# Kernel optimization log

Hardware: AMD Instinct MI355X
Metric: run time of the kernel (lower is better)

Reference implementation:

```python
import jax, jax.numpy as jnp
import numpy as np

K = 1024
DIM = 64
DECAY = 0.99
EPS = 1e-05
CC = 0.25


def setup_inputs() -> dict:
    key = jax.random.key(0)
    k1, k2 = jax.random.split(key)
    inputs = jax.random.normal(k1, (32, DIM, 64, 64), dtype=jnp.float32)
    # embedding initialized uniform(-1/K, 1/K); ema_w starts as a copy
    emb_w = jax.random.uniform(k2, (K, DIM), dtype=jnp.float32, minval=-1.0 / K, maxval=1.0 / K)
    ema_w = emb_w
    ema_cluster_size = jnp.zeros((K,), dtype=jnp.float32)
    return {"inputs": inputs, "emb_w": emb_w, "ema_cluster_size": ema_cluster_size, "ema_w": ema_w}


def reference(inputs, emb_w, ema_cluster_size, ema_w):
    # NCHW -> NHWC
    x = jnp.transpose(inputs, (0, 2, 3, 1))  # [B,H,W,D]
    B, H, W, D = x.shape
    flat = x.reshape(-1, D)  # [N,D]
    # squared L2 distances: |f|^2 - 2 f.W^T + |w|^2
    d = (jnp.sum(flat * flat, axis=1, keepdims=True)
         - 2.0 * flat @ emb_w.T
         + jnp.sum(emb_w * emb_w, axis=1)[None, :])  # [N,K]
    idx = jnp.argmin(d, axis=1)  # [N]
    encodings = idx.reshape(B, H, W)
    quantized = emb_w[idx].reshape(B, H, W, D)

    # training-mode EMA update (matches one_hot.sum(0) and one_hot.T @ flatten)
    counts = jax.ops.segment_sum(jnp.ones_like(idx, dtype=jnp.float32), idx, num_segments=K)
    new_cs = ema_cluster_size * DECAY + (1.0 - DECAY) * counts
    n = jnp.sum(new_cs)
    new_cs = (new_cs + EPS) / (n + K * EPS) * n
    dw = jax.ops.segment_sum(flat, idx, num_segments=K)  # [K,D]
    new_ema_w = ema_w * DECAY + (1.0 - DECAY) * dw
    new_emb_w = new_ema_w / new_cs[:, None]

    e_latent_loss = jnp.mean((quantized - x) ** 2)  # both terms equal in value
    loss = e_latent_loss + CC * e_latent_loss
    # straight-through (value-equal in fwd)
    q_out = jnp.transpose(quantized, (0, 3, 1, 2))  # NHWC -> NCHW
    nll = jnp.ones((1,), dtype=jnp.float32)
    return q_out, encodings, loss, nll, new_cs, new_ema_w, new_emb_w
```

## Files before the change

### kernel.cpp

```cpp
#include <hip/hip_runtime.h>
#include <math.h>

#define KCODES 1024
#define DIMV   64
#define NROWS  131072
#define HWSZ   4096
#define NELEM  8388608
#define CAP    224
#define CANDCAP 1024
#define RPB    128


typedef __attribute__((ext_vector_type(8))) short bf16x8;
typedef __attribute__((ext_vector_type(4))) float f32x4;

static __device__ __forceinline__ unsigned short f2bf(float x) {
    unsigned int u = __float_as_uint(x);
    unsigned int r = (u + 0x7FFFu + ((u >> 16) & 1u)) >> 16;
    return (unsigned short)r;
}

__global__ __launch_bounds__(64) void vq_prep3_kernel(
    const float* __restrict__ emb, float* __restrict__ s_w,
    unsigned short* __restrict__ WB, unsigned int* __restrict__ wmax_bits)
{
    int k = blockIdx.x, t = threadIdx.x;
    float v = emb[k * DIMV + t];

    {
        int cg = k >> 4, n = k & 15;
        int kh = t >> 5, q = (t & 31) >> 3, j = t & 7;
        WB[((cg * 2 + kh) * 4 + q) * 128 + n * 8 + j] = f2bf(v);
    }

    float av = fabsf(v);
    #pragma unroll
    for (int off = 32; off > 0; off >>= 1)
        av = fmaxf(av, __shfl_down(av, off, 64));
    if (t == 0) atomicMax(wmax_bits, __float_as_uint(av));

    __shared__ float sv[64];
    __shared__ float sr[8];
    sv[t] = v;
    __syncthreads();
    if (t < 8) {
        float x = sv[t];
        float sq = x * x;
        asm("" : "+v"(sq));
        float r = sq;
        #pragma unroll
        for (int m = 1; m < 8; ++m) {
            float y = sv[8 * m + t];
            float s2 = y * y;
            asm("" : "+v"(s2));
            r += s2;
        }
        sr[t] = r;
    }
    __syncthreads();
    if (t == 0)
        s_w[k] = ((sr[0] + sr[1]) + (sr[2] + sr[3])) + ((sr[4] + sr[5]) + (sr[6] + sr[7]));
}

__global__ __launch_bounds__(256, 3) void vq_assign_kernel(
    const float* __restrict__ inp, const float* __restrict__ emb,
    const unsigned short* __restrict__ WB, const float* __restrict__ s_w,
    const unsigned int* __restrict__ wmax_bits,
    float* __restrict__ tmp_flat, float* __restrict__ enc_out,
    double* __restrict__ loss_sum, int* __restrict__ counts,
    int* __restrict__ rowlist)
{
    __shared__ float At[RPB * 65];
    __shared__ float sWL[KCODES];
    __shared__ __align__(16) unsigned short Bst[2][2048];
    __shared__ float sfL[RPB];
    __shared__ float errL[RPB];
    __shared__ unsigned long long rowBest[RPB];
    __shared__ int bkL[RPB];
    __shared__ int candL[CANDCAP];
    __shared__ int candCnt;

    const int t = threadIdx.x;
    const int n0 = blockIdx.x * RPB;
    const int bq  = n0 >> 12;
    const int hw0 = n0 & 4095;
    const float* fin = inp + (size_t)bq * (DIMV * HWSZ) + hw0;

    if (t < RPB) rowBest[t] = ~0ULL;
    if (t == 0) candCnt = 0;

    #pragma unroll
    for (int j = 0; j < 4; ++j) sWL[j * 256 + t] = s_w[j * 256 + t];

    #pragma unroll
    for (int j = 0; j < 8; ++j) {
        int id = j * 256 + t;
        int i = id >> 5;
        int c4 = id & 31;
        float4 v = *(const float4*)(fin + (size_t)i * HWSZ + 4 * c4);
        int r = 4 * c4;
        At[(r + 0) * 65 + i] = v.x + v.x;  At[(r + 1) * 65 + i] = v.y + v.y;
        At[(r + 2) * 65 + i] = v.z + v.z;  At[(r + 3) * 65 + i] = v.w + v.w;
    }

    const uint4* wbsrc = (const uint4*)WB;
    uint4 nx0, nx1;
    {
        uint4 st0 = wbsrc[t];
        *(uint4*)&Bst[0][t * 8] = st0;
        nx0 = wbsrc[256 + t];
    }
    __syncthreads();

    if (t < RPB) {
        const float* gr = &At[t * 65];
        float r8[8];
        #pragma unroll
        for (int j = 0; j < 8; ++j) {
            float h = 0.5f * gr[j];
            float sq = h * h;
            asm("" : "+v"(sq));
            r8[j] = sq;
        }
        #pragma unroll
        for (int m = 1; m < 8; ++m) {
            #pragma unroll
            for (int j = 0; j < 8; ++j) {
                float h = 0.5f * gr[8 * m + j];
                float sq = h * h;
                asm("" : "+v"(sq));
                r8[j] += sq;
            }
        }
        sfL[t] = ((r8[0] + r8[1]) + (r8[2] + r8[3])) + ((r8[4] + r8[5]) + (r8[6] + r8[7]));
        float S = 0.0f;
        #pragma unroll
        for (int i = 0; i < 64; ++i) S += fabsf(gr[i]);
        float wmax = __uint_as_float(*wmax_bits);
        errL[t] = fmaf(S * wmax, 0.015625f, 2e-5f);
    }
    __syncthreads();

    const int wv = t >> 6, l = t & 63;
    const int m = l & 15, q = l >> 4;
    const int lq = q * 128 + m * 8;
    bf16x8 afr[2][2];
    float erf[2][4];
    #pragma unroll
    for (int rg2 = 0; rg2 < 2; ++rg2) {
        int row = (2 * wv + rg2) * 16 + m;
        const float* gr = &At[row * 65];
        #pragma unroll
        for (int kh = 0; kh < 2; ++kh) {
            bf16x8 a;
            #pragma unroll
            for (int j = 0; j < 8; ++j)
                a[j] = (short)f2bf(gr[kh * 32 + q * 8 + j]);
            afr[rg2][kh] = a;
        }
        #pragma unroll
        for (int reg = 0; reg < 4; ++reg)
            erf[rg2][reg] = errL[(2 * wv + rg2) * 16 + q * 4 + reg];
    }

    float mn[2][4];
    #pragma unroll
    for (int rg2 = 0; rg2 < 2; ++rg2)
        #pragma unroll
        for (int reg = 0; reg < 4; ++reg) mn[rg2][reg] = 3.0e38f;

    #pragma unroll 1
    for (int tp = 0; tp < 16; ++tp) {
        int tt = 2 * tp;
        nx1 = wbsrc[((tt + 2) & 31) * 256 + t];
        #pragma unroll
        for (int c = 0; c < 2; ++c) {
            int cg = 2 * tt + c;
            bf16x8 b0 = *(const bf16x8*)&Bst[0][c * 1024 + lq];
            bf16x8 b1 = *(const bf16x8*)&Bst[0][c * 1024 + 512 + lq];
            float sw = sWL[cg * 16 + m];
            #pragma unroll
            for (int rg2 = 0; rg2 < 2; ++rg2) {
                f32x4 acc = {0.f, 0.f, 0.f, 0.f};
                acc = __builtin_amdgcn_mfma_f32_16x16x32_bf16(afr[rg2][0], b0, acc, 0, 0, 0);
                acc = __builtin_amdgcn_mfma_f32_16x16x32_bf16(afr[rg2][1], b1, acc, 0, 0, 0);
                #pragma unroll
                for (int reg = 0; reg < 4; ++reg)
                    mn[rg2][reg] = fminf(mn[rg2][reg], sw - acc[reg]);
            }
        }
        *(uint4*)&Bst[1][t * 8] = nx0;
        __syncthreads();
        nx0 = wbsrc[((tt + 3) & 31) * 256 + t];
        #pragma unroll
        for (int c = 0; c < 2; ++c) {
            int cg = 2 * (tt + 1) + c;
            bf16x8 b0 = *(const bf16x8*)&Bst[1][c * 1024 + lq];
            bf16x8 b1 = *(const bf16x8*)&Bst[1][c * 1024 + 512 + lq];
            float sw = sWL[cg * 16 + m];
            #pragma unroll
            for (int rg2 = 0; rg2 < 2; ++rg2) {
                f32x4 acc = {0.f, 0.f, 0.f, 0.f};
                acc = __builtin_amdgcn_mfma_f32_16x16x32_bf16(afr[rg2][0], b0, acc, 0, 0, 0);
                acc = __builtin_amdgcn_mfma_f32_16x16x32_bf16(afr[rg2][1], b1, acc, 0, 0, 0);
                #pragma unroll
                for (int reg = 0; reg < 4; ++reg)
                    mn[rg2][reg] = fminf(mn[rg2][reg], sw - acc[reg]);
            }
        }
        *(uint4*)&Bst[0][t * 8] = nx1;
        __syncthreads();
    }

    float th[2][4];
    #pragma unroll
    for (int rg2 = 0; rg2 < 2; ++rg2)
        #pragma unroll
        for (int reg = 0; reg < 4; ++reg) {
            float v = mn[rg2][reg];
            v = fminf(v, __shfl_xor(v, 1, 64));
            v = fminf(v, __shfl_xor(v, 2, 64));
            v = fminf(v, __shfl_xor(v, 4, 64));
            v = fminf(v, __shfl_xor(v, 8, 64));
            th[rg2][reg] = v + erf[rg2][reg];
        }

    #pragma unroll 1
    for (int tp = 0; tp < 16; ++tp) {
        int tt = 2 * tp;
        nx1 = wbsrc[((tt + 2) & 31) * 256 + t];
        #pragma unroll
        for (int c = 0; c < 2; ++c) {
            int cg = 2 * tt + c;
            bf16x8 b0 = *(const bf16x8*)&Bst[0][c * 1024 + lq];
            bf16x8 b1 = *(const bf16x8*)&Bst[0][c * 1024 + 512 + lq];
            float sw = sWL[cg * 16 + m];
            #pragma unroll
            for (int rg2 = 0; rg2 < 2; ++rg2) {
                f32x4 acc = {0.f, 0.f, 0.f, 0.f};
                acc = __builtin_amdgcn_mfma_f32_16x16x32_bf16(afr[rg2][0], b0, acc, 0, 0, 0);
                acc = __builtin_amdgcn_mfma_f32_16x16x32_bf16(afr[rg2][1], b1, acc, 0, 0, 0);
                #pragma unroll
                for (int reg = 0; reg < 4; ++reg) {
                    if (sw - acc[reg] <= th[rg2][reg]) {
                        int row = (2 * wv + rg2) * 16 + q * 4 + reg;
                        int p = atomicAdd(&candCnt, 1);
                        if (p < CANDCAP) candL[p] = (row << 10) | (cg * 16 + m);
                    }
                }
            }
        }
        *(uint4*)&Bst[1][t * 8] = nx0;
        __syncthreads();
        nx0 = wbsrc[((tt + 3) & 31) * 256 + t];
        #pragma unroll
        for (int c = 0; c < 2; ++c) {
            int cg = 2 * (tt + 1) + c;
            bf16x8 b0 = *(const bf16x8*)&Bst[1][c * 1024 + lq];
            bf16x8 b1 = *(const bf16x8*)&Bst[1][c * 1024 + 512 + lq];
            float sw = sWL[cg * 16 + m];
            #pragma unroll
            for (int rg2 = 0; rg2 < 2; ++rg2) {
                f32x4 acc = {0.f, 0.f, 0.f, 0.f};
                acc = __builtin_amdgcn_mfma_f32_16x16x32_bf16(afr[rg2][0], b0, acc, 0, 0, 0);
                acc = __builtin_amdgcn_mfma_f32_16x16x32_bf16(afr[rg2][1], b1, acc, 0, 0, 0);
                #pragma unroll
                for (int reg = 0; reg < 4; ++reg) {
                    if (sw - acc[reg] <= th[rg2][reg]) {
                        int row = (2 * wv + rg2) * 16 + q * 4 + reg;
                        int p = atomicAdd(&candCnt, 1);
                        if (p < CANDCAP) candL[p] = (row << 10) | (cg * 16 + m);
                    }
                }
            }
        }
        *(uint4*)&Bst[0][t * 8] = nx1;
        __syncthreads();
    }

    int nc = candCnt < CANDCAP ? candCnt : CANDCAP;
    for (int c = t; c < nc; c += 256) {
        int pk = candL[c];
        int r = pk >> 10, k = pk & 1023;
        const float* wk = emb + (size_t)k * DIMV;
        const float* gr = &At[r * 65];
        float acc = 0.0f;
        #pragma unroll
        for (int i = 0; i < DIMV; ++i)
            acc = __builtin_fmaf(gr[i], wk[i], acc);
        float d = (sfL[r] - acc) + sWL[k];
        unsigned int u = __float_as_uint(d);
        unsigned int s = (u & 0x80000000u) ? ~u : (u | 0x80000000u);
        unsigned long long key = ((unsigned long long)s << 32) | (unsigned int)k;
        atomicMin(&rowBest[r], key);
    }
    __syncthreads();

    if (t < RPB && (rowBest[t] == ~0ULL || candCnt > CANDCAP)) {
        int r = t;
        const float* gr = &At[r * 65];
        float bd = 3.0e38f; int bk = 0;
        for (int k = 0; k < KCODES; ++k) {
            const float* wk = emb + (size_t)k * DIMV;
            float acc = 0.0f;
            #pragma unroll
            for (int i = 0; i < DIMV; ++i)
                acc = __builtin_fmaf(gr[i], wk[i], acc);
            float d = (sfL[r] - acc) + sWL[k];
            if (d < bd) { bd = d; bk = k; }
        }
        unsigned int u = __float_as_uint(bd);
        unsigned int s = (u & 0x80000000u) ? ~u : (u | 0x80000000u);
        rowBest[r] = ((unsigned long long)s << 32) | (unsigned int)bk;
    }
    __syncthreads();

    if (t < RPB) {
        int r = t;
        int bk = (int)(rowBest[r] & 1023ULL);
        enc_out[n0 + r] = (float)bk;
        bkL[r] = bk;
        int pos = atomicAdd(&counts[bk], 1);
        if (pos < CAP) rowlist[bk * CAP + pos] = n0 + r;
    }
    __syncthreads();

    float* tq = tmp_flat + (size_t)n0 * DIMV;
    double lsum = 0.0;
    #pragma unroll
    for (int j = 0; j < 32; ++j) {
        int idx = j * 256 + t;
        int r = idx >> 6;
        int i = idx & 63;
        int bk = bkL[r];
        float fi = 0.5f * At[r * 65 + i];
        tq[r * DIMV + i] = fi;
        float qv = emb[bk * DIMV + i];
        double dq = (double)qv - (double)fi;
        lsum = fma(dq, dq, lsum);
    }
    #pragma unroll
    for (int off = 32; off > 0; off >>= 1)
        lsum += __shfl_down(lsum, off, 64);
    if ((t & 63) == 0) atomicAdd(loss_sum, lsum);
}

__global__ __launch_bounds__(256) void vq_dw_all_kernel(
    const float* __restrict__ tmp_flat, const int* __restrict__ rowlist,
    const int* __restrict__ counts, const float* __restrict__ ema_cs,
    const float* __restrict__ ema_w, const double* __restrict__ loss_sum,
    float* __restrict__ out_loss, float* __restrict__ out_nll,
    float* __restrict__ out_ncs, float* __restrict__ out_nema,
    float* __restrict__ out_nemb)
{
    const int k = blockIdx.x;
    const int t = threadIdx.x;
    const double DECAY = 0.99;
    const double OMD   = 1.0 - 0.99;
    const double EPSV  = 1e-5;

    __shared__ double sm[256];
    double part = 0.0;
    #pragma unroll
    for (int j0 = 0; j0 < 4; ++j0) {
        int j = j0 * 256 + t;
        part += (double)ema_cs[j] * DECAY + OMD * (double)counts[j];
    }
    sm[t] = part;
    __syncthreads();
    #pragma unroll
    for (int off = 128; off > 0; off >>= 1) {
        if (t < off) sm[t] += sm[t + off];
        __syncthreads();
    }
    double nsum = sm[0];

    int cnt = counts[k];
    double ncs = (double)ema_cs[k] * DECAY + OMD * (double)cnt;
    double adj = (ncs + EPSV) / (nsum + (double)KCODES * EPSV) * nsum;
    if (t == 0) out_ncs[k] = (float)adj;
    if (k == 0 && t == 0) {
        double e = loss_sum[0] / (double)NELEM;
        out_loss[0] = (float)(e + 0.25 * e);
        out_nll[0]  = 1.0f;
    }

    int i = t & 63;
    int sub = t >> 6;
    int cap = cnt < CAP ? cnt : CAP;

    float acc = 0.0f;
    #pragma unroll 4
    for (int r = sub; r < cap; r += 4) {
        int n = rowlist[k * CAP + r];
        acc += tmp_flat[(size_t)n * DIMV + i];
    }

    __shared__ float red[256];
    red[t] = acc;
    __syncthreads();
    if (t < 128) red[t] += red[t + 128];
    __syncthreads();
    if (t < 64) {
        float dwv = red[t] + red[t + 64];
        int idx = k * DIMV + i;
        double ne = (double)ema_w[idx] * DECAY + OMD * (double)dwv;
        out_nema[idx] = (float)ne;
        out_nemb[idx] = (float)(ne / adj);
    }
}

__global__ __launch_bounds__(256) void vq_qout_kernel(
    const float* __restrict__ enc, const float* __restrict__ emb,
    float* __restrict__ q_out)
{
    __shared__ int bkL[128];
    const int t = threadIdx.x;
    const int n0 = blockIdx.x * 128;
    const int bq  = n0 >> 12;
    const int hw0 = n0 & 4095;
    if (t < 128) bkL[t] = (int)enc[n0 + t];
    __syncthreads();
    float* qo = q_out + (size_t)bq * (DIMV * HWSZ) + hw0;
    #pragma unroll
    for (int j = 0; j < 32; ++j) {
        int idx = j * 256 + t;
        int r = idx & 127;
        int i = idx >> 7;
        qo[(size_t)i * HWSZ + r] = emb[bkL[r] * DIMV + i];
    }
}

extern "C" void kernel_launch(void* const* d_in, const int* in_sizes, int n_in,
                              void* d_out, int out_size, void* d_ws, size_t ws_size,
                              hipStream_t stream) {
    const float* inp    = (const float*)d_in[0];
    const float* emb    = (const float*)d_in[1];
    const float* ema_cs = (const float*)d_in[2];
    const float* ema_w  = (const float*)d_in[3];

    char* ws = (char*)d_ws;
    double*         loss_sum  = (double*)(ws + 0);
    unsigned int*   wmax_bits = (unsigned int*)(ws + 16);
    int*            counts    = (int*)(ws + 32);
    float*          s_w       = (float*)(ws + 4128);
    unsigned short* WB        = (unsigned short*)(ws + 8224);
    int*            rowlist   = (int*)(ws + 139296);

    float* out       = (float*)d_out;
    float* q_out     = out;
    float* enc_out   = out + 8388608;
    float* out_loss  = out + 8519680;
    float* out_nll   = out + 8519681;
    float* out_ncs   = out + 8519682;
    float* out_nema  = out + 8520706;
    float* out_nemb  = out + 8586242;

    hipMemsetAsync(ws, 0, 4128, stream);
    hipLaunchKernelGGL(vq_prep3_kernel, dim3(KCODES), dim3(64), 0, stream,
                       emb, s_w, WB, wmax_bits);
    hipLaunchKernelGGL(vq_assign_kernel, dim3(NROWS / RPB), dim3(256), 0, stream,
                       inp, emb, WB, s_w, wmax_bits,
                       q_out , enc_out, loss_sum, counts, rowlist);
    hipLaunchKernelGGL(vq_dw_all_kernel, dim3(KCODES), dim3(256), 0, stream,
                       q_out , rowlist, counts, ema_cs, ema_w, loss_sum,
                       out_loss, out_nll, out_ncs, out_nema, out_nemb);
    hipLaunchKernelGGL(vq_qout_kernel, dim3(NROWS / 128), dim3(256), 0, stream,
                       enc_out, emb, q_out);
}
```

Measured before the change: 266.4 us.

## Stream codebook tiles with direct global-to-LDS loads and interleave MFMAs

```diff
diff --git a/kernel.cpp b/kernel.cpp
--- a/kernel.cpp
+++ b/kernel.cpp
@@ -13,6 +13,10 @@
 
 typedef __attribute__((ext_vector_type(8))) short bf16x8;
 typedef __attribute__((ext_vector_type(4))) float f32x4;
+
+#define GLD16(gsrc, ldst) __builtin_amdgcn_global_load_lds( \
+    (const __attribute__((address_space(1))) void*)(gsrc),  \
+    (__attribute__((address_space(3))) void*)(ldst), 16, 0, 0)
 
 static __device__ __forceinline__ unsigned short f2bf(float x) {
     unsigned int u = __float_as_uint(x);
@@ -92,6 +96,9 @@
     #pragma unroll
     for (int j = 0; j < 4; ++j) sWL[j * 256 + t] = s_w[j * 256 + t];
 
+    const char* wbByte = (const char*)WB;
+    GLD16(wbByte + t * 16, (char*)&Bst[0][0] + t * 16);
+
     #pragma unroll
     for (int j = 0; j < 8; ++j) {
         int id = j * 256 + t;
@@ -102,14 +109,6 @@
         At[(r + 0) * 65 + i] = v.x + v.x;  At[(r + 1) * 65 + i] = v.y + v.y;
         At[(r + 2) * 65 + i] = v.z + v.z;  At[(r + 3) * 65 + i] = v.w + v.w;
     }
-
-    const uint4* wbsrc = (const uint4*)WB;
-    uint4 nx0, nx1;
-    {
-        uint4 st0 = wbsrc[t];
-        *(uint4*)&Bst[0][t * 8] = st0;
-        nx0 = wbsrc[256 + t];
-    }
     __syncthreads();
 
     if (t < RPB) {
@@ -170,45 +169,33 @@
         for (int reg = 0; reg < 4; ++reg) mn[rg2][reg] = 3.0e38f;
 
     #pragma unroll 1
-    for (int tp = 0; tp < 16; ++tp) {
-        int tt = 2 * tp;
-        nx1 = wbsrc[((tt + 2) & 31) * 256 + t];
-        #pragma unroll
-        for (int c = 0; c < 2; ++c) {
-            int cg = 2 * tt + c;
-            bf16x8 b0 = *(const bf16x8*)&Bst[0][c * 1024 + lq];
-            bf16x8 b1 = *(const bf16x8*)&Bst[0][c * 1024 + 512 + lq];
-            float sw = sWL[cg * 16 + m];
-            #pragma unroll
-            for (int rg2 = 0; rg2 < 2; ++rg2) {
-                f32x4 acc = {0.f, 0.f, 0.f, 0.f};
-                acc = __builtin_amdgcn_mfma_f32_16x16x32_bf16(afr[rg2][0], b0, acc, 0, 0, 0);
-                acc = __builtin_amdgcn_mfma_f32_16x16x32_bf16(afr[rg2][1], b1, acc, 0, 0, 0);
-                #pragma unroll
-                for (int reg = 0; reg < 4; ++reg)
-                    mn[rg2][reg] = fminf(mn[rg2][reg], sw - acc[reg]);
-            }
-        }
-        *(uint4*)&Bst[1][t * 8] = nx0;
-        __syncthreads();
-        nx0 = wbsrc[((tt + 3) & 31) * 256 + t];
-        #pragma unroll
-        for (int c = 0; c < 2; ++c) {
-            int cg = 2 * (tt + 1) + c;
-            bf16x8 b0 = *(const bf16x8*)&Bst[1][c * 1024 + lq];
-            bf16x8 b1 = *(const bf16x8*)&Bst[1][c * 1024 + 512 + lq];
-            float sw = sWL[cg * 16 + m];
-            #pragma unroll
-            for (int rg2 = 0; rg2 < 2; ++rg2) {
-                f32x4 acc = {0.f, 0.f, 0.f, 0.f};
-                acc = __builtin_amdgcn_mfma_f32_16x16x32_bf16(afr[rg2][0], b0, acc, 0, 0, 0);
-                acc = __builtin_amdgcn_mfma_f32_16x16x32_bf16(afr[rg2][1], b1, acc, 0, 0, 0);
-                #pragma unroll
-                for (int reg = 0; reg < 4; ++reg)
-                    mn[rg2][reg] = fminf(mn[rg2][reg], sw - acc[reg]);
-            }
-        }
-        *(uint4*)&Bst[0][t * 8] = nx1;
+    for (int tp = 0; tp < 32; ++tp) {
+        int nxt = (tp + 1) & 31;
+        GLD16(wbByte + nxt * 4096 + t * 16, (char*)&Bst[(tp + 1) & 1][0] + t * 16);
+        const unsigned short* bb = &Bst[tp & 1][0];
+        bf16x8 b00 = *(const bf16x8*)&bb[lq];
+        bf16x8 b01 = *(const bf16x8*)&bb[512 + lq];
+        bf16x8 b10 = *(const bf16x8*)&bb[1024 + lq];
+        bf16x8 b11 = *(const bf16x8*)&bb[1536 + lq];
+        float sw0 = sWL[(2 * tp) * 16 + m];
+        float sw1 = sWL[(2 * tp + 1) * 16 + m];
+        f32x4 t00 = {0.f,0.f,0.f,0.f}, t10 = {0.f,0.f,0.f,0.f};
+        f32x4 t01 = {0.f,0.f,0.f,0.f}, t11 = {0.f,0.f,0.f,0.f};
+        t00 = __builtin_amdgcn_mfma_f32_16x16x32_bf16(afr[0][0], b00, t00, 0, 0, 0);
+        t10 = __builtin_amdgcn_mfma_f32_16x16x32_bf16(afr[1][0], b00, t10, 0, 0, 0);
+        t01 = __builtin_amdgcn_mfma_f32_16x16x32_bf16(afr[0][0], b10, t01, 0, 0, 0);
+        t11 = __builtin_amdgcn_mfma_f32_16x16x32_bf16(afr[1][0], b10, t11, 0, 0, 0);
+        t00 = __builtin_amdgcn_mfma_f32_16x16x32_bf16(afr[0][1], b01, t00, 0, 0, 0);
+        t10 = __builtin_amdgcn_mfma_f32_16x16x32_bf16(afr[1][1], b01, t10, 0, 0, 0);
+        t01 = __builtin_amdgcn_mfma_f32_16x16x32_bf16(afr[0][1], b11, t01, 0, 0, 0);
+        t11 = __builtin_amdgcn_mfma_f32_16x16x32_bf16(afr[1][1], b11, t11, 0, 0, 0);
+        #pragma unroll
+        for (int reg = 0; reg < 4; ++reg) {
+            mn[0][reg] = fminf(mn[0][reg], sw0 - t00[reg]);
+            mn[1][reg] = fminf(mn[1][reg], sw0 - t10[reg]);
+            mn[0][reg] = fminf(mn[0][reg], sw1 - t01[reg]);
+            mn[1][reg] = fminf(mn[1][reg], sw1 - t11[reg]);
+        }
         __syncthreads();
     }
 
@@ -226,55 +213,50 @@
         }
 
     #pragma unroll 1
-    for (int tp = 0; tp < 16; ++tp) {
-        int tt = 2 * tp;
-        nx1 = wbsrc[((tt + 2) & 31) * 256 + t];
-        #pragma unroll
-        for (int c = 0; c < 2; ++c) {
-            int cg = 2 * tt + c;
-            bf16x8 b0 = *(const bf16x8*)&Bst[0][c * 1024 + lq];
-            bf16x8 b1 = *(const bf16x8*)&Bst[0][c * 1024 + 512 + lq];
-            float sw = sWL[cg * 16 + m];
-            #pragma unroll
-            for (int rg2 = 0; rg2 < 2; ++rg2) {
-                f32x4 acc = {0.f, 0.f, 0.f, 0.f};
-                acc = __builtin_amdgcn_mfma_f32_16x16x32_bf16(afr[rg2][0], b0, acc, 0, 0, 0);
-                acc = __builtin_amdgcn_mfma_f32_16x16x32_bf16(afr[rg2][1], b1, acc, 0, 0, 0);
-                #pragma unroll
-                for (int reg = 0; reg < 4; ++reg) {
-                    if (sw - acc[reg] <= th[rg2][reg]) {
-                        int row = (2 * wv + rg2) * 16 + q * 4 + reg;
-                        int p = atomicAdd(&candCnt, 1);
-                        if (p < CANDCAP) candL[p] = (row << 10) | (cg * 16 + m);
-                    }
-                }
+    for (int tp = 0; tp < 32; ++tp) {
+        int nxt = (tp + 1) & 31;
+        GLD16(wbByte + nxt * 4096 + t * 16, (char*)&Bst[(tp + 1) & 1][0] + t * 16);
+        const unsigned short* bb = &Bst[tp & 1][0];
+        bf16x8 b00 = *(const bf16x8*)&bb[lq];
+        bf16x8 b01 = *(const bf16x8*)&bb[512 + lq];
+        bf16x8 b10 = *(const bf16x8*)&bb[1024 + lq];
+        bf16x8 b11 = *(const bf16x8*)&bb[1536 + lq];
+        float sw0 = sWL[(2 * tp) * 16 + m];
+        float sw1 = sWL[(2 * tp + 1) * 16 + m];
+        f32x4 t00 = {0.f,0.f,0.f,0.f}, t10 = {0.f,0.f,0.f,0.f};
+        f32x4 t01 = {0.f,0.f,0.f,0.f}, t11 = {0.f,0.f,0.f,0.f};
+        t00 = __builtin_amdgcn_mfma_f32_16x16x32_bf16(afr[0][0], b00, t00, 0, 0, 0);
+        t10 = __builtin_amdgcn_mfma_f32_16x16x32_bf16(afr[1][0], b00, t10, 0, 0, 0);
+        t01 = __builtin_amdgcn_mfma_f32_16x16x32_bf16(afr[0][0], b10, t01, 0, 0, 0);
+        t11 = __builtin_amdgcn_mfma_f32_16x16x32_bf16(afr[1][0], b10, t11, 0, 0, 0);
+        t00 = __builtin_amdgcn_mfma_f32_16x16x32_bf16(afr[0][1], b01, t00, 0, 0, 0);
+        t10 = __builtin_amdgcn_mfma_f32_16x16x32_bf16(afr[1][1], b01, t10, 0, 0, 0);
+        t01 = __builtin_amdgcn_mfma_f32_16x16x32_bf16(afr[0][1], b11, t01, 0, 0, 0);
+        t11 = __builtin_amdgcn_mfma_f32_16x16x32_bf16(afr[1][1], b11, t11, 0, 0, 0);
+        int cg0 = 2 * tp, cg1 = 2 * tp + 1;
+        #pragma unroll
+        for (int reg = 0; reg < 4; ++reg) {
+            if (sw0 - t00[reg] <= th[0][reg]) {
+                int row = (2 * wv + 0) * 16 + q * 4 + reg;
+                int p = atomicAdd(&candCnt, 1);
+                if (p < CANDCAP) candL[p] = (row << 10) | (cg0 * 16 + m);
             }
-        }
-        *(uint4*)&Bst[1][t * 8] = nx0;
-        __syncthreads();
-        nx0 = wbsrc[((tt + 3) & 31) * 256 + t];
-        #pragma unroll
-        for (int c = 0; c < 2; ++c) {
-            int cg = 2 * (tt + 1) + c;
-            bf16x8 b0 = *(const bf16x8*)&Bst[1][c * 1024 + lq];
-            bf16x8 b1 = *(const bf16x8*)&Bst[1][c * 1024 + 512 + lq];
-            float sw = sWL[cg * 16 + m];
-            #pragma unroll
-            for (int rg2 = 0; rg2 < 2; ++rg2) {
-                f32x4 acc = {0.f, 0.f, 0.f, 0.f};
-                acc = __builtin_amdgcn_mfma_f32_16x16x32_bf16(afr[rg2][0], b0, acc, 0, 0, 0);
-                acc = __builtin_amdgcn_mfma_f32_16x16x32_bf16(afr[rg2][1], b1, acc, 0, 0, 0);
-                #pragma unroll
-                for (int reg = 0; reg < 4; ++reg) {
-                    if (sw - acc[reg] <= th[rg2][reg]) {
-                        int row = (2 * wv + rg2) * 16 + q * 4 + reg;
-                        int p = atomicAdd(&candCnt, 1);
-                        if (p < CANDCAP) candL[p] = (row << 10) | (cg * 16 + m);
-                    }
-                }
+            if (sw0 - t10[reg] <= th[1][reg]) {
+                int row = (2 * wv + 1) * 16 + q * 4 + reg;
+                int p = atomicAdd(&candCnt, 1);
+                if (p < CANDCAP) candL[p] = (row << 10) | (cg0 * 16 + m);
             }
-        }
-        *(uint4*)&Bst[0][t * 8] = nx1;
+            if (sw1 - t01[reg] <= th[0][reg]) {
+                int row = (2 * wv + 0) * 16 + q * 4 + reg;
+                int p = atomicAdd(&candCnt, 1);
+                if (p < CANDCAP) candL[p] = (row << 10) | (cg1 * 16 + m);
+            }
+            if (sw1 - t11[reg] <= th[1][reg]) {
+                int row = (2 * wv + 1) * 16 + q * 4 + reg;
+                int p = atomicAdd(&candCnt, 1);
+                if (p < CANDCAP) candL[p] = (row << 10) | (cg1 * 16 + m);
+            }
+        }
         __syncthreads();
     }
 
```

New measurement: 284.3 us. +6.7%, slower.

## Split codebook across waves and stream bf16 codes from global, dropping LDS staging

Applied to the files above, without the earlier changes.

```diff
diff --git a/kernel.cpp b/kernel.cpp
--- a/kernel.cpp
+++ b/kernel.cpp
@@ -72,9 +72,10 @@
 {
     __shared__ float At[RPB * 65];
     __shared__ float sWL[KCODES];
-    __shared__ __align__(16) unsigned short Bst[2][2048];
     __shared__ float sfL[RPB];
     __shared__ float errL[RPB];
+    __shared__ float thL[RPB];
+    __shared__ float wred[RPB * 4];
     __shared__ unsigned long long rowBest[RPB];
     __shared__ int bkL[RPB];
     __shared__ int candL[CANDCAP];
@@ -102,14 +103,6 @@
         At[(r + 0) * 65 + i] = v.x + v.x;  At[(r + 1) * 65 + i] = v.y + v.y;
         At[(r + 2) * 65 + i] = v.z + v.z;  At[(r + 3) * 65 + i] = v.w + v.w;
     }
-
-    const uint4* wbsrc = (const uint4*)WB;
-    uint4 nx0, nx1;
-    {
-        uint4 st0 = wbsrc[t];
-        *(uint4*)&Bst[0][t * 8] = st0;
-        nx0 = wbsrc[256 + t];
-    }
     __syncthreads();
 
     if (t < RPB) {
@@ -143,12 +136,10 @@
 
     const int wv = t >> 6, l = t & 63;
     const int m = l & 15, q = l >> 4;
-    const int lq = q * 128 + m * 8;
-    bf16x8 afr[2][2];
-    float erf[2][4];
-    #pragma unroll
-    for (int rg2 = 0; rg2 < 2; ++rg2) {
-        int row = (2 * wv + rg2) * 16 + m;
+    bf16x8 afr[8][2];
+    #pragma unroll
+    for (int rg = 0; rg < 8; ++rg) {
+        int row = rg * 16 + m;
         const float* gr = &At[row * 65];
         #pragma unroll
         for (int kh = 0; kh < 2; ++kh) {
@@ -156,127 +147,142 @@
             #pragma unroll
             for (int j = 0; j < 8; ++j)
                 a[j] = (short)f2bf(gr[kh * 32 + q * 8 + j]);
-            afr[rg2][kh] = a;
-        }
-        #pragma unroll
-        for (int reg = 0; reg < 4; ++reg)
-            erf[rg2][reg] = errL[(2 * wv + rg2) * 16 + q * 4 + reg];
-    }
-
-    float mn[2][4];
-    #pragma unroll
-    for (int rg2 = 0; rg2 < 2; ++rg2)
-        #pragma unroll
-        for (int reg = 0; reg < 4; ++reg) mn[rg2][reg] = 3.0e38f;
-
-    #pragma unroll 1
-    for (int tp = 0; tp < 16; ++tp) {
-        int tt = 2 * tp;
-        nx1 = wbsrc[((tt + 2) & 31) * 256 + t];
-        #pragma unroll
-        for (int c = 0; c < 2; ++c) {
-            int cg = 2 * tt + c;
-            bf16x8 b0 = *(const bf16x8*)&Bst[0][c * 1024 + lq];
-            bf16x8 b1 = *(const bf16x8*)&Bst[0][c * 1024 + 512 + lq];
-            float sw = sWL[cg * 16 + m];
-            #pragma unroll
-            for (int rg2 = 0; rg2 < 2; ++rg2) {
+            afr[rg][kh] = a;
+        }
+    }
+
+    const unsigned short* wbw = WB + (wv * 16) * 1024 + q * 128 + m * 8;
+    const int swb0 = wv * 256 + m;
+
+    float mn[8][4];
+    #pragma unroll
+    for (int rg = 0; rg < 8; ++rg)
+        #pragma unroll
+        for (int reg = 0; reg < 4; ++reg) mn[rg][reg] = 3.0e38f;
+
+    {
+        bf16x8 pa0 = *(const bf16x8*)(wbw);
+        bf16x8 pa1 = *(const bf16x8*)(wbw + 512);
+        float   swa = sWL[swb0];
+        bf16x8 pb0 = *(const bf16x8*)(wbw + 1024);
+        bf16x8 pb1 = *(const bf16x8*)(wbw + 1024 + 512);
+        float   swb = sWL[swb0 + 16];
+        for (int cg = 0; cg < 16; cg += 2) {
+            #pragma unroll
+            for (int rg = 0; rg < 8; ++rg) {
                 f32x4 acc = {0.f, 0.f, 0.f, 0.f};
-                acc = __builtin_amdgcn_mfma_f32_16x16x32_bf16(afr[rg2][0], b0, acc, 0, 0, 0);
-                acc = __builtin_amdgcn_mfma_f32_16x16x32_bf16(afr[rg2][1], b1, acc, 0, 0, 0);
+                acc = __builtin_amdgcn_mfma_f32_16x16x32_bf16(afr[rg][0], pa0, acc, 0, 0, 0);
+                acc = __builtin_amdgcn_mfma_f32_16x16x32_bf16(afr[rg][1], pa1, acc, 0, 0, 0);
                 #pragma unroll
                 for (int reg = 0; reg < 4; ++reg)
-                    mn[rg2][reg] = fminf(mn[rg2][reg], sw - acc[reg]);
-            }
-        }
-        *(uint4*)&Bst[1][t * 8] = nx0;
-        __syncthreads();
-        nx0 = wbsrc[((tt + 3) & 31) * 256 + t];
-        #pragma unroll
-        for (int c = 0; c < 2; ++c) {
-            int cg = 2 * (tt + 1) + c;
-            bf16x8 b0 = *(const bf16x8*)&Bst[1][c * 1024 + lq];
-            bf16x8 b1 = *(const bf16x8*)&Bst[1][c * 1024 + 512 + lq];
-            float sw = sWL[cg * 16 + m];
-            #pragma unroll
-            for (int rg2 = 0; rg2 < 2; ++rg2) {
+                    mn[rg][reg] = fminf(mn[rg][reg], swa - acc[reg]);
+            }
+            {
+                int cn = (cg + 2) & 15;
+                pa0 = *(const bf16x8*)(wbw + cn * 1024);
+                pa1 = *(const bf16x8*)(wbw + cn * 1024 + 512);
+                swa = sWL[swb0 + cn * 16];
+            }
+            #pragma unroll
+            for (int rg = 0; rg < 8; ++rg) {
                 f32x4 acc = {0.f, 0.f, 0.f, 0.f};
-                acc = __builtin_amdgcn_mfma_f32_16x16x32_bf16(afr[rg2][0], b0, acc, 0, 0, 0);
-                acc = __builtin_amdgcn_mfma_f32_16x16x32_bf16(afr[rg2][1], b1, acc, 0, 0, 0);
+                acc = __builtin_amdgcn_mfma_f32_16x16x32_bf16(afr[rg][0], pb0, acc, 0, 0, 0);
+                acc = __builtin_amdgcn_mfma_f32_16x16x32_bf16(afr[rg][1], pb1, acc, 0, 0, 0);
                 #pragma unroll
                 for (int reg = 0; reg < 4; ++reg)
-                    mn[rg2][reg] = fminf(mn[rg2][reg], sw - acc[reg]);
-            }
-        }
-        *(uint4*)&Bst[0][t * 8] = nx1;
-        __syncthreads();
-    }
-
-    float th[2][4];
-    #pragma unroll
-    for (int rg2 = 0; rg2 < 2; ++rg2)
+                    mn[rg][reg] = fminf(mn[rg][reg], swb - acc[reg]);
+            }
+            {
+                int cn = (cg + 3) & 15;
+                pb0 = *(const bf16x8*)(wbw + cn * 1024);
+                pb1 = *(const bf16x8*)(wbw + cn * 1024 + 512);
+                swb = sWL[swb0 + cn * 16];
+            }
+        }
+    }
+
+    #pragma unroll
+    for (int rg = 0; rg < 8; ++rg)
         #pragma unroll
         for (int reg = 0; reg < 4; ++reg) {
-            float v = mn[rg2][reg];
+            float v = mn[rg][reg];
             v = fminf(v, __shfl_xor(v, 1, 64));
             v = fminf(v, __shfl_xor(v, 2, 64));
             v = fminf(v, __shfl_xor(v, 4, 64));
             v = fminf(v, __shfl_xor(v, 8, 64));
-            th[rg2][reg] = v + erf[rg2][reg];
-        }
-
-    #pragma unroll 1
-    for (int tp = 0; tp < 16; ++tp) {
-        int tt = 2 * tp;
-        nx1 = wbsrc[((tt + 2) & 31) * 256 + t];
-        #pragma unroll
-        for (int c = 0; c < 2; ++c) {
-            int cg = 2 * tt + c;
-            bf16x8 b0 = *(const bf16x8*)&Bst[0][c * 1024 + lq];
-            bf16x8 b1 = *(const bf16x8*)&Bst[0][c * 1024 + 512 + lq];
-            float sw = sWL[cg * 16 + m];
-            #pragma unroll
-            for (int rg2 = 0; rg2 < 2; ++rg2) {
+            mn[rg][reg] = v;
+        }
+    if (m == 0) {
+        #pragma unroll
+        for (int rg = 0; rg < 8; ++rg)
+            #pragma unroll
+            for (int reg = 0; reg < 4; ++reg)
+                wred[(rg * 16 + q * 4 + reg) * 4 + wv] = mn[rg][reg];
+    }
+    __syncthreads();
+    if (t < RPB)
+        thL[t] = fminf(fminf(wred[t * 4 + 0], wred[t * 4 + 1]),
+                       fminf(wred[t * 4 + 2], wred[t * 4 + 3])) + errL[t];
+    __syncthreads();
+
+    float th[8][4];
+    #pragma unroll
+    for (int rg = 0; rg < 8; ++rg)
+        #pragma unroll
+        for (int reg = 0; reg < 4; ++reg)
+            th[rg][reg] = thL[rg * 16 + q * 4 + reg];
+
+    {
+        bf16x8 pa0 = *(const bf16x8*)(wbw);
+        bf16x8 pa1 = *(const bf16x8*)(wbw + 512);
+        float   swa = sWL[swb0];
+        bf16x8 pb0 = *(const bf16x8*)(wbw + 1024);
+        bf16x8 pb1 = *(const bf16x8*)(wbw + 1024 + 512);
+        float   swb = sWL[swb0 + 16];
+        for (int cg = 0; cg < 16; cg += 2) {
+            #pragma unroll
+            for (int rg = 0; rg < 8; ++rg) {
                 f32x4 acc = {0.f, 0.f, 0.f, 0.f};
-                acc = __builtin_amdgcn_mfma_f32_16x16x32_bf16(afr[rg2][0], b0, acc, 0, 0, 0);
-                acc = __builtin_amdgcn_mfma_f32_16x16x32_bf16(afr[rg2][1], b1, acc, 0, 0, 0);
+                acc = __builtin_amdgcn_mfma_f32_16x16x32_bf16(afr[rg][0], pa0, acc, 0, 0, 0);
+                acc = __builtin_amdgcn_mfma_f32_16x16x32_bf16(afr[rg][1], pa1, acc, 0, 0, 0);
                 #pragma unroll
                 for (int reg = 0; reg < 4; ++reg) {
-                    if (sw - acc[reg] <= th[rg2][reg]) {
-                        int row = (2 * wv + rg2) * 16 + q * 4 + reg;
+                    if (swa - acc[reg] <= th[rg][reg]) {
+                        int row = rg * 16 + q * 4 + reg;
                         int p = atomicAdd(&candCnt, 1);
-                        if (p < CANDCAP) candL[p] = (row << 10) | (cg * 16 + m);
+                        if (p < CANDCAP) candL[p] = (row << 10) | (wv * 256 + cg * 16 + m);
                     }
                 }
             }
-        }
-        *(uint4*)&Bst[1][t * 8] = nx0;
-        __syncthreads();
-        nx0 = wbsrc[((tt + 3) & 31) * 256 + t];
-        #pragma unroll
-        for (int c = 0; c < 2; ++c) {
-            int cg = 2 * (tt + 1) + c;
-            bf16x8 b0 = *(const bf16x8*)&Bst[1][c * 1024 + lq];
-            bf16x8 b1 = *(const bf16x8*)&Bst[1][c * 1024 + 512 + lq];
-            float sw = sWL[cg * 16 + m];
-            #pragma unroll
-            for (int rg2 = 0; rg2 < 2; ++rg2) {
+            {
+                int cn = (cg + 2) & 15;
+                pa0 = *(const bf16x8*)(wbw + cn * 1024);
+                pa1 = *(const bf16x8*)(wbw + cn * 1024 + 512);
+                swa = sWL[swb0 + cn * 16];
+            }
+            #pragma unroll
+            for (int rg = 0; rg < 8; ++rg) {
                 f32x4 acc = {0.f, 0.f, 0.f, 0.f};
-                acc = __builtin_amdgcn_mfma_f32_16x16x32_bf16(afr[rg2][0], b0, acc, 0, 0, 0);
-                acc = __builtin_amdgcn_mfma_f32_16x16x32_bf16(afr[rg2][1], b1, acc, 0, 0, 0);
+                acc = __builtin_amdgcn_mfma_f32_16x16x32_bf16(afr[rg][0], pb0, acc, 0, 0, 0);
+                acc = __builtin_amdgcn_mfma_f32_16x16x32_bf16(afr[rg][1], pb1, acc, 0, 0, 0);
                 #pragma unroll
                 for (int reg = 0; reg < 4; ++reg) {
-                    if (sw - acc[reg] <= th[rg2][reg]) {
-                        int row = (2 * wv + rg2) * 16 + q * 4 + reg;
+                    if (swb - acc[reg] <= th[rg][reg]) {
+                        int row = rg * 16 + q * 4 + reg;
                         int p = atomicAdd(&candCnt, 1);
-                        if (p < CANDCAP) candL[p] = (row << 10) | (cg * 16 + m);
+                        if (p < CANDCAP) candL[p] = (row << 10) | (wv * 256 + (cg + 1) * 16 + m);
                     }
                 }
             }
-        }
-        *(uint4*)&Bst[0][t * 8] = nx1;
-        __syncthreads();
-    }
+            {
+                int cn = (cg + 3) & 15;
+                pb0 = *(const bf16x8*)(wbw + cn * 1024);
+                pb1 = *(const bf16x8*)(wbw + cn * 1024 + 512);
+                swb = sWL[swb0 + cn * 16];
+            }
+        }
+    }
+    __syncthreads();
 
     int nc = candCnt < CANDCAP ? candCnt : CANDCAP;
     for (int c = t; c < nc; c += 256) {
```

Measured after the change: 255.3 us. 1.04x faster.
